# Optimization experiments

Measured on AMD Instinct MI355X. Metric: run time of the kernel, lower is better.

Reference implementation:

```python
import jax, jax.numpy as jnp
import numpy as np

B, L, C = 8, 3136, 192
HEADS, HEAD_CH = 3, 64
EPS = 1e-5


def _dwconv(x, w, s):
    # depthwise 3x3 conv, SAME padding; w: [3,3,1,C], feature_group_count=C
    return jax.lax.conv_general_dilated(
        x, w, (s, s), 'SAME',
        dimension_numbers=('NHWC', 'HWIO', 'NHWC'),
        feature_group_count=x.shape[-1])


def _proj(x, dw, scale, bias, mean, var, pw, s):
    # depthwise conv -> BN (inference, running stats) -> 1x1 pointwise conv
    h = _dwconv(x, dw, s)
    h = (h - mean) * jax.lax.rsqrt(var + EPS) * scale + bias
    return jax.lax.conv_general_dilated(
        h, pw, (1, 1), 'SAME',
        dimension_numbers=('NHWC', 'HWIO', 'NHWC'))


def setup_inputs() -> dict:
    key = jax.random.key(0)
    ks = jax.random.split(key, 7)
    d = {'x': jax.random.normal(ks[0], (B, L, C), jnp.float32)}
    for i, p in enumerate(['q', 'k', 'v']):
        d[p + '_dw'] = jax.random.normal(ks[i + 1], (3, 3, 1, C), jnp.float32) * 0.1
        d[p + '_scale'] = jnp.ones((C,), jnp.float32)
        d[p + '_bias'] = jnp.zeros((C,), jnp.float32)
        d[p + '_mean'] = jnp.zeros((C,), jnp.float32)
        d[p + '_var'] = jnp.ones((C,), jnp.float32)
        d[p + '_pw'] = jax.random.normal(ks[i + 4], (1, 1, C, HEADS * HEAD_CH), jnp.float32) * 0.05
    d['is_training'] = 0  # inference: BN uses running averages
    return d


def reference(x, q_dw, q_scale, q_bias, q_mean, q_var, q_pw,
              k_dw, k_scale, k_bias, k_mean, k_var, k_pw,
              v_dw, v_scale, v_bias, v_mean, v_var, v_pw,
              is_training):
    S = int(np.ceil(np.sqrt(L)))  # 56; L is a perfect square, so no token padding
    xi = x.reshape(B, S, S, C)
    q = _proj(xi, q_dw, q_scale, q_bias, q_mean, q_var, q_pw, 1)  # [B,56,56,192]
    k = _proj(xi, k_dw, k_scale, k_bias, k_mean, k_var, k_pw, 2)  # [B,28,28,192]
    v = _proj(xi, v_dw, v_scale, v_bias, v_mean, v_var, v_pw, 2)  # [B,28,28,192]
    q = q.reshape(B, -1, HEADS, HEAD_CH) / jnp.sqrt(jnp.float32(HEAD_CH))
    k = k.reshape(B, -1, HEADS, HEAD_CH)
    v = v.reshape(B, -1, HEADS, HEAD_CH)
    attn = jax.nn.softmax(jnp.einsum('bqhd,bkhd->bhqk', q, k), axis=-1)
    o = jnp.einsum('bhqk,bkhd->bqhd', attn, v)
    # num_heads*head_ch == out_ch -> plain head merge, no output projection
    return o.reshape(B, L, HEADS * HEAD_CH)
```

## Files before the change

kernel.cpp:

```cpp
#include <hip/hip_runtime.h>
#include <cmath>

#define EPS_BN 1e-5f

typedef __bf16 bf16;
typedef __bf16 bf16x4 __attribute__((ext_vector_type(4)));
typedef __bf16 bf16x8 __attribute__((ext_vector_type(8)));
typedef float  f32x4  __attribute__((ext_vector_type(4)));

__device__ __forceinline__ void dma16(const bf16* g, bf16* l) {
    __builtin_amdgcn_global_load_lds(
        (const __attribute__((address_space(1))) void*)g,
        (__attribute__((address_space(3))) void*)l, 16, 0, 0);
}

__global__ __launch_bounds__(256) void conv_all_kernel(
    const float* __restrict__ x,
    const float* __restrict__ qdw, const float* __restrict__ qscale,
    const float* __restrict__ qbias, const float* __restrict__ qmean,
    const float* __restrict__ qvar,
    const float* __restrict__ kdw, const float* __restrict__ kscale,
    const float* __restrict__ kbias, const float* __restrict__ kmean,
    const float* __restrict__ kvar,
    const float* __restrict__ vdw, const float* __restrict__ vscale,
    const float* __restrict__ vbias, const float* __restrict__ vmean,
    const float* __restrict__ vvar,
    const float* __restrict__ qpw, const float* __restrict__ kpw,
    const float* __restrict__ vpw,
    bf16* __restrict__ qhi, bf16* __restrict__ qlo,
    bf16* __restrict__ khi, bf16* __restrict__ klo,
    bf16* __restrict__ vhi, bf16* __restrict__ vlo,
    bf16* __restrict__ wt) {
    const int WW = 56, C = 192;
    int bid = blockIdx.x;

    if (bid < 4704) {
        int idx = bid * 256 + threadIdx.x;
        int p  = idx / 48;
        int c4 = (idx - p * 48) * 4;
        int b  = p / 3136;
        int rem = p - b * 3136;
        int oy = rem / 56;
        int ox = rem - oy * 56;
        const float* xb = x + (size_t)b * 3136 * C;

        float4 sc = *(const float4*)&qscale[c4];
        float4 vr = *(const float4*)&qvar[c4];
        float4 bi = *(const float4*)&qbias[c4];
        float4 mn = *(const float4*)&qmean[c4];
        float aA[4] = {sc.x * rsqrtf(vr.x + EPS_BN), sc.y * rsqrtf(vr.y + EPS_BN),
                       sc.z * rsqrtf(vr.z + EPS_BN), sc.w * rsqrtf(vr.w + EPS_BN)};
        float aB[4] = {bi.x - mn.x * aA[0], bi.y - mn.y * aA[1],
                       bi.z - mn.z * aA[2], bi.w - mn.w * aA[3]};
        float s[4] = {0.f, 0.f, 0.f, 0.f};
#pragma unroll
        for (int ky = 0; ky < 3; ky++) {
            int iy = oy + ky - 1;
            bool yok = (iy >= 0) && (iy < 56);
#pragma unroll
            for (int kx = 0; kx < 3; kx++) {
                int ix = ox + kx - 1;
                if (yok && ix >= 0 && ix < WW) {
                    float4 xv = *(const float4*)&xb[((size_t)iy * WW + ix) * C + c4];
                    float4 wv = *(const float4*)&qdw[(ky * 3 + kx) * C + c4];
                    s[0] += xv.x * wv.x; s[1] += xv.y * wv.y;
                    s[2] += xv.z * wv.z; s[3] += xv.w * wv.w;
                }
            }
        }
        bf16x4 hv, lv;
#pragma unroll
        for (int j = 0; j < 4; j++) {
            float av = s[j] * aA[j] + aB[j];
            bf16 hh = (bf16)av;
            hv[j] = hh;
            lv[j] = (bf16)(av - (float)hh);
        }
        *(bf16x4*)&qhi[(size_t)p * C + c4] = hv;
        *(bf16x4*)&qlo[(size_t)p * C + c4] = lv;
    } else if (bid < 5880) {
        int idx = (bid - 4704) * 256 + threadIdx.x;
        int p  = idx / 48;
        int c4 = (idx - p * 48) * 4;
        int b  = p / 784;
        int rem = p - b * 784;
        int oy = rem / 28;
        int ox = rem - oy * 28;
        const float* xb = x + (size_t)b * 3136 * C;

        float ks[4] = {0.f, 0.f, 0.f, 0.f};
        float vs[4] = {0.f, 0.f, 0.f, 0.f};
#pragma unroll
        for (int ky = 0; ky < 3; ky++) {
            int iy = oy * 2 + ky;
            bool yok = iy < 56;
#pragma unroll
            for (int kx = 0; kx < 3; kx++) {
                int ix = ox * 2 + kx;
                if (yok && ix < WW) {
                    float4 xv = *(const float4*)&xb[((size_t)iy * WW + ix) * C + c4];
                    float4 kw = *(const float4*)&kdw[(ky * 3 + kx) * C + c4];
                    float4 vw = *(const float4*)&vdw[(ky * 3 + kx) * C + c4];
                    ks[0] += xv.x * kw.x; ks[1] += xv.y * kw.y;
                    ks[2] += xv.z * kw.z; ks[3] += xv.w * kw.w;
                    vs[0] += xv.x * vw.x; vs[1] += xv.y * vw.y;
                    vs[2] += xv.z * vw.z; vs[3] += xv.w * vw.w;
                }
            }
        }
        float4 ksc = *(const float4*)&kscale[c4];
        float4 kvr = *(const float4*)&kvar[c4];
        float4 kbi = *(const float4*)&kbias[c4];
        float4 kmn = *(const float4*)&kmean[c4];
        float4 vsc = *(const float4*)&vscale[c4];
        float4 vvr = *(const float4*)&vvar[c4];
        float4 vbi = *(const float4*)&vbias[c4];
        float4 vmn = *(const float4*)&vmean[c4];
        float kA[4] = {ksc.x * rsqrtf(kvr.x + EPS_BN), ksc.y * rsqrtf(kvr.y + EPS_BN),
                       ksc.z * rsqrtf(kvr.z + EPS_BN), ksc.w * rsqrtf(kvr.w + EPS_BN)};
        float kB[4] = {kbi.x - kmn.x * kA[0], kbi.y - kmn.y * kA[1],
                       kbi.z - kmn.z * kA[2], kbi.w - kmn.w * kA[3]};
        float vA[4] = {vsc.x * rsqrtf(vvr.x + EPS_BN), vsc.y * rsqrtf(vvr.y + EPS_BN),
                       vsc.z * rsqrtf(vvr.z + EPS_BN), vsc.w * rsqrtf(vvr.w + EPS_BN)};
        float vB[4] = {vbi.x - vmn.x * vA[0], vbi.y - vmn.y * vA[1],
                       vbi.z - vmn.z * vA[2], vbi.w - vmn.w * vA[3]};
        bf16x4 kh, kl, vh, vl;
#pragma unroll
        for (int j = 0; j < 4; j++) {
            float kf = ks[j] * kA[j] + kB[j];
            float vf = vs[j] * vA[j] + vB[j];
            bf16 h1 = (bf16)kf; kh[j] = h1; kl[j] = (bf16)(kf - (float)h1);
            bf16 h2 = (bf16)vf; vh[j] = h2; vl[j] = (bf16)(vf - (float)h2);
        }
        *(bf16x4*)&khi[(size_t)p * C + c4] = kh;
        *(bf16x4*)&klo[(size_t)p * C + c4] = kl;
        *(bf16x4*)&vhi[(size_t)p * C + c4] = vh;
        *(bf16x4*)&vlo[(size_t)p * C + c4] = vl;
    } else {
        int idx = (bid - 5880) * 256 + threadIdx.x;
        if (idx < 3 * 36864) {
            int mat = idx / 36864, r = idx % 36864;
            int n = r / 192, k = r - n * 192;
            const float* src = (mat == 0) ? qpw : (mat == 1) ? kpw : vpw;
            wt[idx] = (bf16)src[k * 192 + n];
        }
    }
}

__global__ __launch_bounds__(256) void gemm_all_kernel(
    const bf16* __restrict__ qhi, const bf16* __restrict__ qlo,
    const bf16* __restrict__ khi, const bf16* __restrict__ klo,
    const bf16* __restrict__ vhi, const bf16* __restrict__ vlo,
    const bf16* __restrict__ wt,
    bf16* __restrict__ qbuf, bf16* __restrict__ kbuf, bf16* __restrict__ vtbuf) {
    __shared__ bf16 Ws[96][200];
    int t = threadIdx.x;
    int bid = blockIdx.x;

    int mode, mt, nh;
    const bf16 *Ahi, *Alo, *Wsrc;
    if (bid < 784)      { mode = 0; mt = bid >> 1;         nh = bid & 1;
                          Ahi = qhi; Alo = qlo; Wsrc = wt; }
    else if (bid < 980) { mode = 1; int r = bid - 784; mt = r >> 1; nh = r & 1;
                          Ahi = khi; Alo = klo; Wsrc = wt + 36864; }
    else                { mode = 2; int r = bid - 980; mt = r >> 1; nh = r & 1;
                          Ahi = vhi; Alo = vlo; Wsrc = wt + 73728; }
    int n0 = nh * 96;

#pragma unroll
    for (int it = 0; it < 9; it++) {
        int idx = it * 256 + t;
        int n = idx / 24, ck = idx - n * 24;
        *(uint4*)&Ws[n][ck * 8] = *(const uint4*)&Wsrc[(size_t)(n0 + n) * 192 + ck * 8];
    }
    __syncthreads();

    int lane = t & 63, wid = t >> 6;
    int l16 = lane & 15, quad = lane >> 4;
    int wrow = wid * 16;
    int m0 = mt * 64;

    f32x4 acc[6];
#pragma unroll
    for (int n = 0; n < 6; n++) acc[n] = f32x4{0.f, 0.f, 0.f, 0.f};

    const bf16* arh = Ahi + (size_t)(m0 + wrow + l16) * 192;
    const bf16* arl = Alo + (size_t)(m0 + wrow + l16) * 192;
#pragma unroll
    for (int kc = 0; kc < 6; kc++) {
        bf16x8 ah = *(const bf16x8*)(arh + kc * 32 + quad * 8);
        bf16x8 al = *(const bf16x8*)(arl + kc * 32 + quad * 8);
#pragma unroll
        for (int n = 0; n < 6; n++) {
            bf16x8 bfr = *(const bf16x8*)&Ws[n * 16 + l16][kc * 32 + quad * 8];
            acc[n] = __builtin_amdgcn_mfma_f32_16x16x32_bf16(al, bfr, acc[n], 0, 0, 0);
            acc[n] = __builtin_amdgcn_mfma_f32_16x16x32_bf16(ah, bfr, acc[n], 0, 0, 0);
        }
    }

    if (mode == 2) {
#pragma unroll
        for (int reg = 0; reg < 4; reg++) {
            int row = m0 + wrow + quad * 4 + reg;
            int b = row / 784;
            int loc = row - b * 784;
#pragma unroll
            for (int n = 0; n < 6; n++) {
                int col = n0 + n * 16 + l16;
                int h = col >> 6, d = col & 63;
                vtbuf[(((size_t)b * 3 + h) * 64 + d) * 784 + loc] = (bf16)acc[n][reg];
            }
        }
    } else {
        bf16* outp = (mode == 0) ? qbuf : kbuf;
        const float s = (mode == 0) ? 0.125f : 1.0f;
#pragma unroll
        for (int reg = 0; reg < 4; reg++) {
            size_t row = m0 + wrow + quad * 4 + reg;
#pragma unroll
            for (int n = 0; n < 6; n++)
                outp[row * 192 + n0 + n * 16 + l16] = (bf16)(acc[n][reg] * s);
        }
    }
}

__global__ __launch_bounds__(256)
__attribute__((amdgpu_waves_per_eu(2, 2)))
void attn3_kernel(const bf16* __restrict__ qb,
                  const bf16* __restrict__ kb,
                  const bf16* __restrict__ vtb,
                  float* __restrict__ out) {
    const int LQ = 3136, LK = 784, C = 192;
    int qt = blockIdx.x, h = blockIdx.y, b = blockIdx.z;

    __shared__ bf16 Ks[2][7168];
    __shared__ bf16 Vts[8192];
    __shared__ bf16 Ps[64][136];

    int t    = threadIdx.x;
    int lane = t & 63;
    int wid  = t >> 6;
    int l16  = lane & 15;
    int quad = lane >> 4;
    int wrow = wid * 16;

    if (lane < 32) {
        int row = wrow + (lane >> 1);
        int part = lane & 1;
        *(uint4*)&Ps[row][112 + part * 8] = make_uint4(0u, 0u, 0u, 0u);
    }

    const bf16* kbase  = kb + (size_t)b * LK * C + h * 64;
    const bf16* vtbase = vtb + ((size_t)(b * 3 + h)) * 64 * LK;

    const bf16* ksrc = kbase + (lane >> 3) * C + (((lane & 7) ^ (lane >> 3)) * 8);

    int voff[4];
#pragma unroll
    for (int i = 0; i < 4; i++) {
        int s = wid + 4 * i;
        int j = s * 64 + lane;
        int row = j >> 4;
        int l = (j & 15) ^ (row & 7);
        voff[i] = row * LK + l * 8;
    }

    for (int s = wid; s < 14; s += 4)
        dma16(ksrc + s * 8 * C, &Ks[0][s * 512]);

    bf16x8 qfrag[2];
    {
        const bf16* qrow = qb + ((size_t)b * LQ + qt * 64 + wrow + l16) * C + h * 64;
        qfrag[0] = *(const bf16x8*)(qrow + quad * 8);
        qfrag[1] = *(const bf16x8*)(qrow + 32 + quad * 8);
    }

    int kA0 = l16 * 64 + (((quad    ) ^ (l16 & 7)) * 8);
    int kA1 = l16 * 64 + (((quad + 4) ^ (l16 & 7)) * 8);

    float m_run = -INFINITY, l_run = 0.f;
    f32x4 o_acc[4];
#pragma unroll
    for (int dt = 0; dt < 4; dt++) o_acc[dt] = f32x4{0.f, 0.f, 0.f, 0.f};

    __syncthreads();

    for (int c = 0; c < 7; c++) {
        const int cur = c & 1, nxt = cur ^ 1;
        const int j0 = c * 112;

#pragma unroll
        for (int i = 0; i < 4; i++)
            dma16(vtbase + j0 + voff[i], Vts + (wid + 4 * i) * 512);
        __builtin_amdgcn_sched_barrier(0);

        if (c < 6) {
            const bf16* kn = ksrc + (size_t)(c + 1) * 112 * C;
            for (int s = wid; s < 14; s += 4)
                dma16(kn + s * 8 * C, &Ks[nxt][s * 512]);
        }
        __builtin_amdgcn_sched_barrier(0);

        f32x4 st[7];
#pragma unroll
        for (int kb7 = 0; kb7 < 7; kb7++) st[kb7] = f32x4{0.f, 0.f, 0.f, 0.f};
#pragma unroll
        for (int kk = 0; kk < 2; kk++) {
            int kA = (kk == 0) ? kA0 : kA1;
#pragma unroll
            for (int kb7 = 0; kb7 < 7; kb7++) {
                bf16x8 afrag = *(const bf16x8*)&Ks[cur][kb7 * 1024 + kA];
                st[kb7] = __builtin_amdgcn_mfma_f32_16x16x32_bf16(afrag, qfrag[kk], st[kb7], 0, 0, 0);
            }
        }

        float mx = -INFINITY;
#pragma unroll
        for (int kb7 = 0; kb7 < 7; kb7++)
#pragma unroll
            for (int r = 0; r < 4; r++) mx = fmaxf(mx, st[kb7][r]);
        mx = fmaxf(mx, __shfl_xor(mx, 16, 64));
        mx = fmaxf(mx, __shfl_xor(mx, 32, 64));
        float m_new = fmaxf(m_run, mx);
        float alpha = __expf(m_run - m_new);

        float rs = 0.f;
#pragma unroll
        for (int kb7 = 0; kb7 < 7; kb7++) {
            bf16x4 pv;
#pragma unroll
            for (int r = 0; r < 4; r++) {
                float p = __expf(st[kb7][r] - m_new);
                rs += p;
                pv[r] = (bf16)p;
            }
            *(bf16x4*)&Ps[wrow + l16][kb7 * 16 + quad * 4] = pv;
        }
        rs += __shfl_xor(rs, 16, 64);
        rs += __shfl_xor(rs, 32, 64);
        l_run = l_run * alpha + rs;
        m_run = m_new;
#pragma unroll
        for (int dt = 0; dt < 4; dt++)
#pragma unroll
            for (int r = 0; r < 4; r++) o_acc[dt][r] *= alpha;

        if (c < 6) {
            if (wid < 2) asm volatile("s_waitcnt vmcnt(4)" ::: "memory");
            else         asm volatile("s_waitcnt vmcnt(3)" ::: "memory");
        } else {
            asm volatile("s_waitcnt vmcnt(0)" ::: "memory");
        }
        __builtin_amdgcn_s_barrier();
        __builtin_amdgcn_sched_barrier(0);

        int vx = l16 & 7;
#pragma unroll
        for (int kk = 0; kk < 4; kk++) {
            bf16x8 pfrag = *(const bf16x8*)&Ps[wrow + l16][kk * 32 + quad * 8];
#pragma unroll
            for (int dt = 0; dt < 4; dt++) {
                bf16x8 vfrag = *(const bf16x8*)&Vts[(dt * 16 + l16) * 128
                                                   + (((kk * 4 + quad) ^ vx) * 8)];
                o_acc[dt] = __builtin_amdgcn_mfma_f32_16x16x32_bf16(vfrag, pfrag, o_acc[dt], 0, 0, 0);
            }
        }

        __syncthreads();
    }

    float invl = 1.f / l_run;
    float* ob = out + ((size_t)b * LQ + qt * 64 + wrow + l16) * C + h * 64;
#pragma unroll
    for (int dt = 0; dt < 4; dt++) {
        float4 v4 = {o_acc[dt][0] * invl, o_acc[dt][1] * invl,
                     o_acc[dt][2] * invl, o_acc[dt][3] * invl};
        *(float4*)(ob + dt * 16 + quad * 4) = v4;
    }
}

extern "C" void kernel_launch(void* const* d_in, const int* in_sizes, int n_in,
                              void* d_out, int out_size, void* d_ws, size_t ws_size,
                              hipStream_t stream) {
    const float* x = (const float*)d_in[0];

    const float* q_dw = (const float*)d_in[1];
    const float* q_scale = (const float*)d_in[2];
    const float* q_bias = (const float*)d_in[3];
    const float* q_mean = (const float*)d_in[4];
    const float* q_var = (const float*)d_in[5];
    const float* q_pw = (const float*)d_in[6];

    const float* k_dw = (const float*)d_in[7];
    const float* k_scale = (const float*)d_in[8];
    const float* k_bias = (const float*)d_in[9];
    const float* k_mean = (const float*)d_in[10];
    const float* k_var = (const float*)d_in[11];
    const float* k_pw = (const float*)d_in[12];

    const float* v_dw = (const float*)d_in[13];
    const float* v_scale = (const float*)d_in[14];
    const float* v_bias = (const float*)d_in[15];
    const float* v_mean = (const float*)d_in[16];
    const float* v_var = (const float*)d_in[17];
    const float* v_pw = (const float*)d_in[18];

    float* out = (float*)d_out;

    char* ws = (char*)d_ws;
    bf16* qhi = (bf16*)(ws);
    bf16* qlo = (bf16*)(ws + 9633792);
    bf16* khi = (bf16*)(ws + 19267584);
    bf16* klo = (bf16*)(ws + 21676032);
    bf16* vhi = (bf16*)(ws + 24084480);
    bf16* vlo = (bf16*)(ws + 26492928);
    bf16* qbuf = (bf16*)(ws + 28901376);
    bf16* kbuf = (bf16*)(ws + 38535168);
    bf16* vtbuf = (bf16*)(ws + 40943616);
    bf16* wt = (bf16*)(ws + 43352064);

    conv_all_kernel<<<6312, 256, 0, stream>>>(
        x,
        q_dw, q_scale, q_bias, q_mean, q_var,
        k_dw, k_scale, k_bias, k_mean, k_var,
        v_dw, v_scale, v_bias, v_mean, v_var,
        q_pw, k_pw, v_pw,
        qhi, qlo, khi, klo, vhi, vlo, wt);

    gemm_all_kernel<<<1176, 256, 0, stream>>>(
        qhi, qlo, khi, klo, vhi, vlo, wt, qbuf, kbuf, vtbuf);

    attn3_kernel<<<dim3(49, 3, 8), 256, 0, stream>>>(qbuf, kbuf, vtbuf, out);
}
```

Before: 184.2 us.

## Shrink P staging buffer with XOR swizzle and raise attention occupancy to 3 waves

The P tile in LDS shrinks from 64x136 to a 64x64 XOR-swizzled buffer. Probabilities are now held in registers and written in two halves, each consumed by half of the PV MFMAs, with the tail columns zeroed explicitly. Together with the smaller LDS footprint, the waves-per-EU hint rises from 2 to 3 so more blocks fit per CU and can hide latency. The cost is extra registers for the packed P values and tighter register limits, which could cause spills. Reusing the buffer between halves also relies on each wave touching only its own rows, with no barrier in between.

```diff
diff --git a/kernel.cpp b/kernel.cpp
--- a/kernel.cpp
+++ b/kernel.cpp
@@ -225,7 +225,7 @@
 }
 
 __global__ __launch_bounds__(256)
-__attribute__((amdgpu_waves_per_eu(2, 2)))
+__attribute__((amdgpu_waves_per_eu(3, 3)))
 void attn3_kernel(const bf16* __restrict__ qb,
                   const bf16* __restrict__ kb,
                   const bf16* __restrict__ vtb,
@@ -235,7 +235,7 @@
 
     __shared__ bf16 Ks[2][7168];
     __shared__ bf16 Vts[8192];
-    __shared__ bf16 Ps[64][136];
+    __shared__ bf16 Ps[4096];
 
     int t    = threadIdx.x;
     int lane = t & 63;
@@ -243,12 +243,8 @@
     int l16  = lane & 15;
     int quad = lane >> 4;
     int wrow = wid * 16;
-
-    if (lane < 32) {
-        int row = wrow + (lane >> 1);
-        int part = lane & 1;
-        *(uint4*)&Ps[row][112 + part * 8] = make_uint4(0u, 0u, 0u, 0u);
-    }
+    int l7   = l16 & 7;
+    int qh   = quad >> 1;
 
     const bf16* kbase  = kb + (size_t)b * LK * C + h * 64;
     const bf16* vtbase = vtb + ((size_t)(b * 3 + h)) * 64 * LK;
@@ -275,8 +271,11 @@
         qfrag[1] = *(const bf16x8*)(qrow + 32 + quad * 8);
     }
 
-    int kA0 = l16 * 64 + (((quad    ) ^ (l16 & 7)) * 8);
-    int kA1 = l16 * 64 + (((quad + 4) ^ (l16 & 7)) * 8);
+    int kA0 = l16 * 64 + (((quad    ) ^ l7) * 8);
+    int kA1 = l16 * 64 + (((quad + 4) ^ l7) * 8);
+
+    int prow   = (wrow + l16) * 64;
+    int pwbase = prow + (quad & 1) * 4;
 
     float m_run = -INFINITY, l_run = 0.f;
     f32x4 o_acc[4];
@@ -325,6 +324,7 @@
         float alpha = __expf(m_run - m_new);
 
         float rs = 0.f;
+        bf16x4 pk[7];
 #pragma unroll
         for (int kb7 = 0; kb7 < 7; kb7++) {
             bf16x4 pv;
@@ -334,7 +334,7 @@
                 rs += p;
                 pv[r] = (bf16)p;
             }
-            *(bf16x4*)&Ps[wrow + l16][kb7 * 16 + quad * 4] = pv;
+            pk[kb7] = pv;
         }
         rs += __shfl_xor(rs, 16, 64);
         rs += __shfl_xor(rs, 32, 64);
@@ -344,6 +344,10 @@
         for (int dt = 0; dt < 4; dt++)
 #pragma unroll
             for (int r = 0; r < 4; r++) o_acc[dt][r] *= alpha;
+
+#pragma unroll
+        for (int kb = 0; kb < 4; kb++)
+            *(bf16x4*)&Ps[pwbase + (((kb * 2 + qh) ^ l7) * 8)] = pk[kb];
 
         if (c < 6) {
             if (wid < 2) asm volatile("s_waitcnt vmcnt(4)" ::: "memory");
@@ -354,14 +358,32 @@
         __builtin_amdgcn_s_barrier();
         __builtin_amdgcn_sched_barrier(0);
 
-        int vx = l16 & 7;
-#pragma unroll
-        for (int kk = 0; kk < 4; kk++) {
-            bf16x8 pfrag = *(const bf16x8*)&Ps[wrow + l16][kk * 32 + quad * 8];
+#pragma unroll
+        for (int kk = 0; kk < 2; kk++) {
+            bf16x8 pfrag = *(const bf16x8*)&Ps[prow + (((kk * 4 + quad) ^ l7) * 8)];
 #pragma unroll
             for (int dt = 0; dt < 4; dt++) {
                 bf16x8 vfrag = *(const bf16x8*)&Vts[(dt * 16 + l16) * 128
-                                                   + (((kk * 4 + quad) ^ vx) * 8)];
+                                                   + (((kk * 4 + quad) ^ l7) * 8)];
+                o_acc[dt] = __builtin_amdgcn_mfma_f32_16x16x32_bf16(vfrag, pfrag, o_acc[dt], 0, 0, 0);
+            }
+        }
+
+#pragma unroll
+        for (int kb = 0; kb < 3; kb++)
+            *(bf16x4*)&Ps[pwbase + (((kb * 2 + qh) ^ l7) * 8)] = pk[4 + kb];
+        {
+            bf16x4 zv = {(bf16)0.f, (bf16)0.f, (bf16)0.f, (bf16)0.f};
+            *(bf16x4*)&Ps[pwbase + (((6 + qh) ^ l7) * 8)] = zv;
+        }
+
+#pragma unroll
+        for (int kk = 2; kk < 4; kk++) {
+            bf16x8 pfrag = *(const bf16x8*)&Ps[prow + ((((kk - 2) * 4 + quad) ^ l7) * 8)];
+#pragma unroll
+            for (int dt = 0; dt < 4; dt++) {
+                bf16x8 vfrag = *(const bf16x8*)&Vts[(dt * 16 + l16) * 128
+                                                   + (((kk * 4 + quad) ^ l7) * 8)];
                 o_acc[dt] = __builtin_amdgcn_mfma_f32_16x16x32_bf16(vfrag, pfrag, o_acc[dt], 0, 0, 0);
             }
         }
```

Result: faster. 176.6 us (-4.2%).

## Shrink attention key chunks to 80 to fit four waves per EU

Applied to the files above, without the earlier changes.

The attention kernel now processes keys in 10 chunks of 80 instead of 7 chunks of 112. This cuts LDS for K, V^T and P and raises the occupancy target from 2 to 4 waves per EU. The P staging buffer becomes a small per-wave scratch that is written and reread for each 32-key slice, and the V^T tile drops its XOR swizzle in favour of a padded 104-element row stride. s_setprio hints are also added around the MFMA sections. The risks are more loop iterations and barriers, bank conflicts from the unswizzled V reads, and tighter register limits at the higher occupancy.

```diff
diff --git a/kernel.cpp b/kernel.cpp
--- a/kernel.cpp
+++ b/kernel.cpp
@@ -225,7 +225,7 @@
 }
 
 __global__ __launch_bounds__(256)
-__attribute__((amdgpu_waves_per_eu(2, 2)))
+__attribute__((amdgpu_waves_per_eu(4, 4)))
 void attn3_kernel(const bf16* __restrict__ qb,
                   const bf16* __restrict__ kb,
                   const bf16* __restrict__ vtb,
@@ -233,9 +233,9 @@
     const int LQ = 3136, LK = 784, C = 192;
     int qt = blockIdx.x, h = blockIdx.y, b = blockIdx.z;
 
-    __shared__ bf16 Ks[2][7168];
-    __shared__ bf16 Vts[8192];
-    __shared__ bf16 Ps[64][136];
+    __shared__ bf16 Ks[2][5120];
+    __shared__ bf16 Vts[6656];
+    __shared__ bf16 Ps[2560];
 
     int t    = threadIdx.x;
     int lane = t & 63;
@@ -243,12 +243,7 @@
     int l16  = lane & 15;
     int quad = lane >> 4;
     int wrow = wid * 16;
-
-    if (lane < 32) {
-        int row = wrow + (lane >> 1);
-        int part = lane & 1;
-        *(uint4*)&Ps[row][112 + part * 8] = make_uint4(0u, 0u, 0u, 0u);
-    }
+    int l7   = l16 & 7;
 
     const bf16* kbase  = kb + (size_t)b * LK * C + h * 64;
     const bf16* vtbase = vtb + ((size_t)(b * 3 + h)) * 64 * LK;
@@ -259,13 +254,14 @@
 #pragma unroll
     for (int i = 0; i < 4; i++) {
         int s = wid + 4 * i;
-        int j = s * 64 + lane;
-        int row = j >> 4;
-        int l = (j & 15) ^ (row & 7);
-        voff[i] = row * LK + l * 8;
-    }
-
-    for (int s = wid; s < 14; s += 4)
+        int jc = s * 64 + lane;
+        int row = jc / 13;
+        int cc = jc - row * 13;
+        int key8 = (cc < 10) ? cc * 8 : 72;
+        voff[i] = (s < 13) ? (row * LK + key8) : 0;
+    }
+
+    for (int s = wid; s < 10; s += 4)
         dma16(ksrc + s * 8 * C, &Ks[0][s * 512]);
 
     bf16x8 qfrag[2];
@@ -275,8 +271,9 @@
         qfrag[1] = *(const bf16x8*)(qrow + 32 + quad * 8);
     }
 
-    int kA0 = l16 * 64 + (((quad    ) ^ (l16 & 7)) * 8);
-    int kA1 = l16 * 64 + (((quad + 4) ^ (l16 & 7)) * 8);
+    int kA0 = l16 * 64 + (((quad    ) ^ l7) * 8);
+    int kA1 = l16 * 64 + (((quad + 4) ^ l7) * 8);
+    int prow = (wrow + l16) * 40;
 
     float m_run = -INFINITY, l_run = 0.f;
     f32x4 o_acc[4];
@@ -285,56 +282,63 @@
 
     __syncthreads();
 
-    for (int c = 0; c < 7; c++) {
+    for (int c = 0; c < 10; c++) {
         const int cur = c & 1, nxt = cur ^ 1;
-        const int j0 = c * 112;
-
-#pragma unroll
-        for (int i = 0; i < 4; i++)
-            dma16(vtbase + j0 + voff[i], Vts + (wid + 4 * i) * 512);
+        const int j0 = c * 80;
+
+#pragma unroll
+        for (int i = 0; i < 4; i++) {
+            int s = wid + 4 * i;
+            if (s < 13) dma16(vtbase + j0 + voff[i], Vts + s * 512);
+        }
         __builtin_amdgcn_sched_barrier(0);
 
-        if (c < 6) {
-            const bf16* kn = ksrc + (size_t)(c + 1) * 112 * C;
-            for (int s = wid; s < 14; s += 4)
+        if (c < 9) {
+            const bf16* kn = ksrc + (size_t)(c + 1) * 80 * C;
+            for (int s = wid; s < 10; s += 4)
                 dma16(kn + s * 8 * C, &Ks[nxt][s * 512]);
         }
         __builtin_amdgcn_sched_barrier(0);
 
-        f32x4 st[7];
-#pragma unroll
-        for (int kb7 = 0; kb7 < 7; kb7++) st[kb7] = f32x4{0.f, 0.f, 0.f, 0.f};
+        f32x4 st[5];
+#pragma unroll
+        for (int kb5 = 0; kb5 < 5; kb5++) st[kb5] = f32x4{0.f, 0.f, 0.f, 0.f};
+        __builtin_amdgcn_s_setprio(1);
 #pragma unroll
         for (int kk = 0; kk < 2; kk++) {
             int kA = (kk == 0) ? kA0 : kA1;
 #pragma unroll
-            for (int kb7 = 0; kb7 < 7; kb7++) {
-                bf16x8 afrag = *(const bf16x8*)&Ks[cur][kb7 * 1024 + kA];
-                st[kb7] = __builtin_amdgcn_mfma_f32_16x16x32_bf16(afrag, qfrag[kk], st[kb7], 0, 0, 0);
-            }
-        }
+            for (int kb5 = 0; kb5 < 5; kb5++) {
+                bf16x8 afrag = *(const bf16x8*)&Ks[cur][kb5 * 1024 + kA];
+                st[kb5] = __builtin_amdgcn_mfma_f32_16x16x32_bf16(afrag, qfrag[kk], st[kb5], 0, 0, 0);
+            }
+        }
+        __builtin_amdgcn_s_setprio(0);
+
+        if (c == 9) st[4] = f32x4{-1e30f, -1e30f, -1e30f, -1e30f};
 
         float mx = -INFINITY;
 #pragma unroll
-        for (int kb7 = 0; kb7 < 7; kb7++)
-#pragma unroll
-            for (int r = 0; r < 4; r++) mx = fmaxf(mx, st[kb7][r]);
+        for (int kb5 = 0; kb5 < 5; kb5++)
+#pragma unroll
+            for (int r = 0; r < 4; r++) mx = fmaxf(mx, st[kb5][r]);
         mx = fmaxf(mx, __shfl_xor(mx, 16, 64));
         mx = fmaxf(mx, __shfl_xor(mx, 32, 64));
         float m_new = fmaxf(m_run, mx);
         float alpha = __expf(m_run - m_new);
 
         float rs = 0.f;
-#pragma unroll
-        for (int kb7 = 0; kb7 < 7; kb7++) {
+        bf16x4 pk[5];
+#pragma unroll
+        for (int kb5 = 0; kb5 < 5; kb5++) {
             bf16x4 pv;
 #pragma unroll
             for (int r = 0; r < 4; r++) {
-                float p = __expf(st[kb7][r] - m_new);
+                float p = __expf(st[kb5][r] - m_new);
                 rs += p;
                 pv[r] = (bf16)p;
             }
-            *(bf16x4*)&Ps[wrow + l16][kb7 * 16 + quad * 4] = pv;
+            pk[kb5] = pv;
         }
         rs += __shfl_xor(rs, 16, 64);
         rs += __shfl_xor(rs, 32, 64);
@@ -345,25 +349,33 @@
 #pragma unroll
             for (int r = 0; r < 4; r++) o_acc[dt][r] *= alpha;
 
-        if (c < 6) {
-            if (wid < 2) asm volatile("s_waitcnt vmcnt(4)" ::: "memory");
-            else         asm volatile("s_waitcnt vmcnt(3)" ::: "memory");
+        if (c < 9) {
+            if (wid < 2) asm volatile("s_waitcnt vmcnt(3)" ::: "memory");
+            else         asm volatile("s_waitcnt vmcnt(2)" ::: "memory");
         } else {
             asm volatile("s_waitcnt vmcnt(0)" ::: "memory");
         }
         __builtin_amdgcn_s_barrier();
         __builtin_amdgcn_sched_barrier(0);
 
-        int vx = l16 & 7;
-#pragma unroll
-        for (int kk = 0; kk < 4; kk++) {
-            bf16x8 pfrag = *(const bf16x8*)&Ps[wrow + l16][kk * 32 + quad * 8];
+        bf16x4 zv = {(bf16)0.f, (bf16)0.f, (bf16)0.f, (bf16)0.f};
+#pragma unroll
+        for (int kk = 0; kk < 3; kk++) {
+            bf16x4 w1;
+            if (kk == 0)      w1 = pk[1];
+            else if (kk == 1) w1 = pk[3];
+            else              w1 = zv;
+            *(bf16x4*)&Ps[prow + quad * 4]      = pk[2 * kk];
+            *(bf16x4*)&Ps[prow + 16 + quad * 4] = w1;
+            bf16x8 pfrag = *(const bf16x8*)&Ps[prow + quad * 8];
+            __builtin_amdgcn_s_setprio(1);
 #pragma unroll
             for (int dt = 0; dt < 4; dt++) {
-                bf16x8 vfrag = *(const bf16x8*)&Vts[(dt * 16 + l16) * 128
-                                                   + (((kk * 4 + quad) ^ vx) * 8)];
+                bf16x8 vfrag = *(const bf16x8*)&Vts[(dt * 16 + l16) * 104
+                                                   + (kk * 4 + quad) * 8];
                 o_acc[dt] = __builtin_amdgcn_mfma_f32_16x16x32_bf16(vfrag, pfrag, o_acc[dt], 0, 0, 0);
             }
+            __builtin_amdgcn_s_setprio(0);
         }
 
         __syncthreads();
```

Result: no change. 184.3 us (+0.0%).
